# Kernel tuning notes

Measured on AMD Instinct MI355X. Metric: run time of the kernel, lower is better.

Reference implementation:

```python
import jax, jax.numpy as jnp
import numpy as np

NUM_USER = 30000
NUM_ITEM = 30000
N = NUM_USER + NUM_ITEM
DIM = 64          # dim_latent
HID = 4 * DIM     # MLP hidden = 4*dim_latent
E_PAIRS = 500000  # user-item interactions; symmetrized -> 2*E_PAIRS edges
K = 10            # sampling (user-graph neighbors)
B = 2048          # batch_size
DV, DA, DT = 1024, 128, 100


def setup_inputs() -> dict:
    key = jax.random.key(0)
    ks = jax.random.split(key, 24)
    src = jax.random.randint(ks[0], (E_PAIRS,), 0, NUM_USER)
    dst = jax.random.randint(ks[1], (E_PAIRS,), NUM_USER, N)
    # symmetrize like torch.cat((edge, edge[[1,0]]), dim=1)
    edge_index = jnp.stack([jnp.concatenate([src, dst]),
                            jnp.concatenate([dst, src])])  # [2, 2*E_PAIRS]

    def lin_w(k, o, i):
        s = 1.0 / np.sqrt(i)
        return jax.random.uniform(k, (o, i), minval=-s, maxval=s, dtype=jnp.float32)

    return {
        "user_nodes": jax.random.randint(ks[2], (B,), 0, NUM_USER),
        "pos_item_nodes": jax.random.randint(ks[3], (B,), NUM_USER, N),
        "neg_item_nodes": jax.random.randint(ks[4], (B,), NUM_USER, N),
        "user_graph": jax.random.randint(ks[5], (NUM_USER, K), 0, NUM_USER),
        "edge_index": edge_index,
        "user_weight_matrix": jax.nn.softmax(jax.random.normal(ks[6], (NUM_USER, K), dtype=jnp.float32), axis=-1),
        "v_feat": jax.random.normal(ks[7], (NUM_ITEM, DV), dtype=jnp.float32),
        "a_feat": jax.random.normal(ks[8], (NUM_ITEM, DA), dtype=jnp.float32),
        "t_feat": jax.random.normal(ks[9], (NUM_ITEM, DT), dtype=jnp.float32),
        "v_pref": 0.1 * jax.random.normal(ks[10], (NUM_USER, DIM), dtype=jnp.float32),
        "a_pref": 0.1 * jax.random.normal(ks[11], (NUM_USER, DIM), dtype=jnp.float32),
        "t_pref": 0.1 * jax.random.normal(ks[12], (NUM_USER, DIM), dtype=jnp.float32),
        "v_W1": lin_w(ks[13], HID, DV), "v_b1": jnp.zeros((HID,), jnp.float32),
        "v_W2": lin_w(ks[14], DIM, HID), "v_b2": jnp.zeros((DIM,), jnp.float32),
        "a_W1": lin_w(ks[15], HID, DA), "a_b1": jnp.zeros((HID,), jnp.float32),
        "a_W2": lin_w(ks[16], DIM, HID), "a_b2": jnp.zeros((DIM,), jnp.float32),
        "t_W1": lin_w(ks[17], HID, DT), "t_b1": jnp.zeros((HID,), jnp.float32),
        "t_W2": lin_w(ks[18], DIM, HID), "t_b2": jnp.zeros((DIM,), jnp.float32),
        "weight_u": jax.nn.softmax(jax.random.normal(ks[19], (NUM_USER, 3, 1), dtype=jnp.float32), axis=1),
    }


def _l2norm(x):
    # F.normalize(x): rowwise L2 with eps=1e-12
    return x / jnp.maximum(jnp.linalg.norm(x, axis=-1, keepdims=True), 1e-12)


def _gcn_conv(x, src, dst, dinv):
    # Base_gcn(aggr='add'): out[i] = sum_{e: dst_e=i} dinv[src_e]*dinv[dst_e]*x[src_e]
    norm = dinv[src] * dinv[dst]
    return jax.ops.segment_sum(norm[:, None] * x[src], dst, num_segments=N)


def _modality(feat, pref, W1, b1, W2, b2, src, dst, dinv):
    # GCN.forward (Movielens branch, dim_latent=64)
    temp = jax.nn.leaky_relu(feat @ W1.T + b1) @ W2.T + b2  # MLP_1(leaky_relu(MLP(f)))
    x = _l2norm(jnp.concatenate([pref, temp], axis=0))       # [N, DIM]
    h = _gcn_conv(x, src, dst, dinv)
    h1 = _gcn_conv(h, src, dst, dinv)
    return h + x + h1


def reference(user_nodes, pos_item_nodes, neg_item_nodes, user_graph, edge_index,
              user_weight_matrix, v_feat, a_feat, t_feat,
              v_pref, a_pref, t_pref,
              v_W1, v_b1, v_W2, v_b2,
              a_W1, a_b1, a_W2, a_b2,
              t_W1, t_b1, t_W2, t_b2, weight_u):
    src, dst = edge_index[0], edge_index[1]
    deg = jax.ops.segment_sum(jnp.ones_like(src, dtype=jnp.float32), src, num_segments=N)
    dinv = jnp.where(deg > 0, deg ** -0.5, 0.0)

    v_rep = _modality(v_feat, v_pref, v_W1, v_b1, v_W2, v_b2, src, dst, dinv)
    a_rep = _modality(a_feat, a_pref, a_W1, a_b1, a_W2, a_b2, src, dst, dinv)
    t_rep = _modality(t_feat, t_pref, t_W1, t_b1, t_W2, t_b2, src, dst, dinv)

    representation = (v_rep + a_rep + t_rep) / 3.0
    # weighted_sum construction: per-user learned modality weights [U,3,1]
    user_stack = jnp.stack([v_rep[:NUM_USER], a_rep[:NUM_USER], t_rep[:NUM_USER]], axis=2)  # [U, D, 3]
    user_rep = jnp.einsum('udm,umo->ud', user_stack, weight_u)
    item_rep = representation[NUM_USER:]

    # User_Graph_sample: weighted sum over k sampled user neighbors
    h_u1 = jnp.einsum('uk,ukd->ud', user_weight_matrix, user_rep[user_graph])
    user_rep = user_rep + h_u1

    result = jnp.concatenate([user_rep, item_rep], axis=0)  # [N, DIM]
    u = result[user_nodes]
    pos_scores = jnp.sum(u * result[pos_item_nodes], axis=1)
    neg_scores = jnp.sum(u * result[neg_item_nodes], axis=1)
    return pos_scores, neg_scores
```

## Files before the change

kernel.cpp:

```cpp
#include <hip/hip_runtime.h>
#include <hip/hip_bf16.h>
#include <math.h>

#define NUSER 30000
#define NITEM 30000
#define NN    60000
#define NE    1000000
#define DIMV  64
#define XW    192
#define HIDW  256
#define NB    2048
#define KNB   10
#define MPAD  30080
#define NCH   235

typedef __attribute__((ext_vector_type(8))) short bf16x8;
typedef __attribute__((ext_vector_type(4))) float f32x4;

__device__ __forceinline__ short f2bf(float f) {
    union { float f; unsigned u; } v; v.f = f;
    unsigned r = v.u + 0x7fff + ((v.u >> 16) & 1);
    return (short)(r >> 16);
}
__device__ __forceinline__ float bflo(unsigned v) { return __int_as_float(v << 16); }
__device__ __forceinline__ float bfhi(unsigned v) { return __int_as_float(v & 0xffff0000u); }
__device__ __forceinline__ unsigned pack2(float a, float b) {
    return (unsigned)(unsigned short)f2bf(a) | ((unsigned)(unsigned short)f2bf(b) << 16);
}
__device__ __forceinline__ void async16(void* lds, const void* g) {
    __builtin_amdgcn_global_load_lds(
        (const __attribute__((address_space(1))) unsigned*)g,
        (__attribute__((address_space(3))) unsigned*)lds, 16, 0, 0);
}

__global__ void k_deg(const int* __restrict__ src, unsigned* __restrict__ deg) {
    int e = blockIdx.x * blockDim.x + threadIdx.x;
    if (e < NE) atomicAdd(&deg[src[e]], 1u);
}
__global__ void k_dinv(const unsigned* __restrict__ deg, float* __restrict__ dinv) {
    int i = blockIdx.x * blockDim.x + threadIdx.x;
    if (i < NN) { unsigned d = deg[i]; dinv[i] = d ? rsqrtf((float)d) : 0.f; }
}
__global__ __launch_bounds__(256)
void k_bsum(const unsigned* __restrict__ deg, int* __restrict__ bsum) {
    __shared__ int red[4];
    int g = blockIdx.x * 256 + threadIdx.x;
    int v = (g < NN) ? (int)deg[g] : 0;
    for (int o = 32; o > 0; o >>= 1) v += __shfl_down(v, o);
    int lane = threadIdx.x & 63, wave = threadIdx.x >> 6;
    if (lane == 0) red[wave] = v;
    __syncthreads();
    if (threadIdx.x == 0) bsum[blockIdx.x] = red[0] + red[1] + red[2] + red[3];
}
__global__ __launch_bounds__(256)
void k_bscan(const int* __restrict__ bsum, int* __restrict__ bscan) {
    __shared__ int s[256];
    int t = threadIdx.x;
    int v = (t < NCH) ? bsum[t] : 0;
    s[t] = v;
    __syncthreads();
    for (int o = 1; o < 256; o <<= 1) {
        int u = (t >= o) ? s[t - o] : 0;
        __syncthreads();
        s[t] += u;
        __syncthreads();
    }
    if (t < NCH) bscan[t] = s[t] - v;
}
__global__ __launch_bounds__(256)
void k_rowptr(const unsigned* __restrict__ deg, const int* __restrict__ bscan,
              int* __restrict__ rowptr) {
    __shared__ int s[256];
    int g = blockIdx.x * 256 + threadIdx.x, t = threadIdx.x;
    int v = (g < NN) ? (int)deg[g] : 0;
    s[t] = v;
    __syncthreads();
    for (int o = 1; o < 256; o <<= 1) {
        int u = (t >= o) ? s[t - o] : 0;
        __syncthreads();
        s[t] += u;
        __syncthreads();
    }
    int base = bscan[blockIdx.x];
    if (g < NN) rowptr[g] = base + s[t] - v;
    if (g == NN - 1) rowptr[NN] = base + s[t];
}
__global__ void k_fill(const int* __restrict__ src, const int* __restrict__ dst,
                       const float* __restrict__ dinv, const int* __restrict__ rowptr,
                       unsigned* __restrict__ cursor, int2* __restrict__ csr) {
    int e = blockIdx.x * blockDim.x + threadIdx.x;
    if (e >= NE) return;
    int s = src[e], d = dst[e];
    int pos = (int)atomicAdd(&cursor[d], 1u);
    int2 ew;
    ew.x = s;
    ew.y = __float_as_int(dinv[s] * dinv[d]);
    csr[rowptr[d] + pos] = ew;
}

struct CvtArgs { const float* src[9]; short* dst[9]; };
__constant__ __device__ const int C8PRE[10] = {0,3850240,4331520,4812800,4845568,
                                               4849664,4853760,4855808,4857856,4859904};
__constant__ __device__ const int C8SH[9]   = {7,4,4,7,4,4,5,5,5};
__constant__ __device__ const int C8COLS[9] = {1024,128,100,1024,128,100,256,256,256};
__constant__ __device__ const int C8ROWS[9] = {30000,30000,30000,256,256,256,64,64,64};
#define CVT8_TOTAL 4859904

__global__ __launch_bounds__(256)
void k_convert(CvtArgs a) {
    int cid = blockIdx.x * 256 + threadIdx.x;
    if (cid >= CVT8_TOTAL) return;
    int j = 0;
    while (cid >= C8PRE[j + 1]) ++j;
    int local = cid - C8PRE[j];
    int sh = C8SH[j];
    int r = local >> sh;
    int col = (local & ((1 << sh) - 1)) * 8;
    int cols = C8COLS[j];
    bf16x8 o = (bf16x8)0;
    if (r < C8ROWS[j]) {
        const float* s = a.src[j] + (size_t)r * cols + col;
        if (col + 8 <= cols) {
            float4 f0 = *(const float4*)s;
            float4 f1 = *(const float4*)(s + 4);
            o[0] = f2bf(f0.x); o[1] = f2bf(f0.y); o[2] = f2bf(f0.z); o[3] = f2bf(f0.w);
            o[4] = f2bf(f1.x); o[5] = f2bf(f1.y); o[6] = f2bf(f1.z); o[7] = f2bf(f1.w);
        } else {
            #pragma unroll
            for (int q = 0; q < 8; ++q)
                if (col + q < cols) o[q] = f2bf(s[q]);
        }
    }
    *(bf16x8*)(a.dst[j] + ((size_t)r << (sh + 3)) + col) = o;
}

__device__ __forceinline__ bf16x8 ldfrag(const short* lds, int row, int kbyte) {
    int off = (row * 128 + kbyte) ^ ((row & 7) << 4);
    return *(const bf16x8*)((const char*)lds + off);
}
#define STAGE_TILE(SMEM, BASEPTR, LDK, ROWOFF, K0, NITERS)                          \
    _Pragma("unroll")                                                                \
    for (int i_ = 0; i_ < (NITERS); ++i_) {                                          \
        int c_ = i_ * 256 + wave * 64 + lane;                                        \
        int r_ = c_ >> 3, slot_ = c_ & 7;                                            \
        int ss_ = slot_ ^ (r_ & 7);                                                  \
        const char* gp_ = (const char*)((BASEPTR) + (size_t)((ROWOFF) + r_) * (LDK)  \
                                        + (K0)) + ss_ * 16;                          \
        async16(&(SMEM)[(i_ * 256 + wave * 64) * 8], gp_);                           \
    }

struct G1Args { const short* A[3]; const short* W[3]; const float* bias[3];
                short* C[3]; int K[3]; };
__global__ __launch_bounds__(256)
void gemm1_mfma(G1Args g) {
    __shared__ __align__(16) short sA[128 * 64];
    __shared__ __align__(16) short sB[128 * 64];
    int m = blockIdx.z;
    int K = g.K[m];
    const short* A = g.A[m];
    const short* W = g.W[m];
    int lane = threadIdx.x & 63, wave = threadIdx.x >> 6;
    int wr = wave >> 1, wc = wave & 1;
    int lane15 = lane & 15, lhi = lane >> 4;
    int row0 = blockIdx.x * 128, col0 = blockIdx.y * 128;
    f32x4 acc[4][4] = {};
    for (int t = 0; t < (K >> 6); ++t) {
        int k0 = t * 64;
        STAGE_TILE(sA, A, K, row0, k0, 4)
        STAGE_TILE(sB, W, K, col0, k0, 4)
        __syncthreads();
        #pragma unroll
        for (int ks = 0; ks < 2; ++ks) {
            int kb = ks * 64 + lhi * 16;
            bf16x8 a[4], b[4];
            #pragma unroll
            for (int mi = 0; mi < 4; ++mi) a[mi] = ldfrag(sA, wr * 64 + mi * 16 + lane15, kb);
            #pragma unroll
            for (int ni = 0; ni < 4; ++ni) b[ni] = ldfrag(sB, wc * 64 + ni * 16 + lane15, kb);
            #pragma unroll
            for (int mi = 0; mi < 4; ++mi)
                #pragma unroll
                for (int ni = 0; ni < 4; ++ni)
                    acc[mi][ni] = __builtin_amdgcn_mfma_f32_16x16x32_bf16(a[mi], b[ni], acc[mi][ni], 0, 0, 0);
        }
        __syncthreads();
    }
    short* C = g.C[m];
    const float* bias = g.bias[m];
    #pragma unroll
    for (int mi = 0; mi < 4; ++mi) {
        int grow0 = row0 + wr * 64 + mi * 16 + lhi * 4;
        #pragma unroll
        for (int ni = 0; ni < 4; ++ni) {
            int gcol = col0 + wc * 64 + ni * 16 + lane15;
            float bv = bias[gcol];
            #pragma unroll
            for (int r = 0; r < 4; ++r) {
                float v = acc[mi][ni][r] + bv;
                v = v > 0.f ? v : 0.01f * v;
                C[(size_t)(grow0 + r) * HIDW + gcol] = f2bf(v);
            }
        }
    }
}

struct G2Args { const short* A[3]; const short* W[3]; const float* bias[3]; };
__global__ __launch_bounds__(256)
void gemm2_mfma(G2Args g, float* __restrict__ X, short* __restrict__ Xb) {
    __shared__ __align__(16) short sA[128 * 64];
    __shared__ __align__(16) short sB[64 * 64];
    int m = blockIdx.z;
    const short* A = g.A[m];
    const short* W = g.W[m];
    int lane = threadIdx.x & 63, wave = threadIdx.x >> 6;
    int lane15 = lane & 15, lhi = lane >> 4;
    int row0 = blockIdx.x * 128;
    const int K = HIDW;
    f32x4 acc[2][4] = {};
    for (int t = 0; t < 4; ++t) {
        int k0 = t * 64;
        STAGE_TILE(sA, A, K, row0, k0, 4)
        STAGE_TILE(sB, W, K, 0, k0, 2)
        __syncthreads();
        #pragma unroll
        for (int ks = 0; ks < 2; ++ks) {
            int kb = ks * 64 + lhi * 16;
            bf16x8 a[2], b[4];
            #pragma unroll
            for (int mi = 0; mi < 2; ++mi) a[mi] = ldfrag(sA, wave * 32 + mi * 16 + lane15, kb);
            #pragma unroll
            for (int ni = 0; ni < 4; ++ni) b[ni] = ldfrag(sB, ni * 16 + lane15, kb);
            #pragma unroll
            for (int mi = 0; mi < 2; ++mi)
                #pragma unroll
                for (int ni = 0; ni < 4; ++ni)
                    acc[mi][ni] = __builtin_amdgcn_mfma_f32_16x16x32_bf16(a[mi], b[ni], acc[mi][ni], 0, 0, 0);
        }
        __syncthreads();
    }
    const float* bias = g.bias[m];
    #pragma unroll
    for (int mi = 0; mi < 2; ++mi) {
        float v[4][4];
        float sumsq[4] = {};
        #pragma unroll
        for (int ni = 0; ni < 4; ++ni) {
            float bv = bias[ni * 16 + lane15];
            #pragma unroll
            for (int r = 0; r < 4; ++r) {
                float x = acc[mi][ni][r] + bv;
                v[ni][r] = x;
                sumsq[r] += x * x;
            }
        }
        #pragma unroll
        for (int r = 0; r < 4; ++r) {
            float s = sumsq[r];
            s += __shfl_xor(s, 1); s += __shfl_xor(s, 2);
            s += __shfl_xor(s, 4); s += __shfl_xor(s, 8);
            sumsq[r] = 1.f / fmaxf(sqrtf(s), 1e-12f);
        }
        int grow0 = row0 + wave * 32 + mi * 16 + lhi * 4;
        #pragma unroll
        for (int r = 0; r < 4; ++r) {
            int grow = grow0 + r;
            if (grow < NITEM) {
                float sc = sumsq[r];
                size_t o = (size_t)(NUSER + grow) * XW + m * DIMV;
                #pragma unroll
                for (int ni = 0; ni < 4; ++ni) {
                    float val = v[ni][r] * sc;
                    X[o + ni * 16 + lane15] = val;
                    Xb[o + ni * 16 + lane15] = f2bf(val);
                }
            }
        }
    }
}

__global__ void k_users_norm(const float* __restrict__ vp, const float* __restrict__ ap,
                             const float* __restrict__ tp, float* __restrict__ X,
                             short* __restrict__ Xb) {
    int gw = (blockIdx.x * blockDim.x + threadIdx.x) >> 6;
    int lane = threadIdx.x & 63;
    if (gw >= NUSER * 3) return;
    int u = gw / 3, m = gw % 3;
    const float* p = (m == 0) ? vp : (m == 1) ? ap : tp;
    float v = p[(size_t)u * DIMV + lane];
    float s = v * v;
    for (int o = 32; o > 0; o >>= 1) s += __shfl_xor(s, o);
    float sc = 1.f / fmaxf(sqrtf(s), 1e-12f);
    size_t o = (size_t)u * XW + m * DIMV + lane;
    float val = v * sc;
    X[o] = val;
    Xb[o] = f2bf(val);
}

template<int MODE>
__global__ __launch_bounds__(256)
void k_spmm(const int* __restrict__ rowptr, const int2* __restrict__ csr,
            const short* __restrict__ INB, const float* __restrict__ Xf,
            float* __restrict__ OUTf, short* __restrict__ OUTB) {
    int n = blockIdx.x * 4 + (threadIdx.x >> 6);
    int l = threadIdx.x & 63;
    if (n >= NN) return;
    int lo = rowptr[n], hi = rowptr[n + 1];
    int lc = l < 48 ? l : 47;
    float f0 = 0.f, f1 = 0.f, f2 = 0.f, f3 = 0.f;
    for (int base = lo; base < hi; base += 64) {
        int idx = base + l;
        int2 e = (idx < hi) ? csr[idx] : make_int2(0, 0);
        int m = hi - base; if (m > 64) m = 64;
        int j = 0;
        for (; j + 4 <= m; j += 4) {
            int s0 = __builtin_amdgcn_readlane(e.x, j + 0);
            int s1 = __builtin_amdgcn_readlane(e.x, j + 1);
            int s2 = __builtin_amdgcn_readlane(e.x, j + 2);
            int s3 = __builtin_amdgcn_readlane(e.x, j + 3);
            float w0 = __int_as_float(__builtin_amdgcn_readlane(e.y, j + 0));
            float w1 = __int_as_float(__builtin_amdgcn_readlane(e.y, j + 1));
            float w2 = __int_as_float(__builtin_amdgcn_readlane(e.y, j + 2));
            float w3 = __int_as_float(__builtin_amdgcn_readlane(e.y, j + 3));
            uint2 v0 = ((const uint2*)(INB + (size_t)s0 * XW))[lc];
            uint2 v1 = ((const uint2*)(INB + (size_t)s1 * XW))[lc];
            uint2 v2 = ((const uint2*)(INB + (size_t)s2 * XW))[lc];
            uint2 v3 = ((const uint2*)(INB + (size_t)s3 * XW))[lc];
            f0 += w0 * bflo(v0.x); f1 += w0 * bfhi(v0.x);
            f2 += w0 * bflo(v0.y); f3 += w0 * bfhi(v0.y);
            f0 += w1 * bflo(v1.x); f1 += w1 * bfhi(v1.x);
            f2 += w1 * bflo(v1.y); f3 += w1 * bfhi(v1.y);
            f0 += w2 * bflo(v2.x); f1 += w2 * bfhi(v2.x);
            f2 += w2 * bflo(v2.y); f3 += w2 * bfhi(v2.y);
            f0 += w3 * bflo(v3.x); f1 += w3 * bfhi(v3.x);
            f2 += w3 * bflo(v3.y); f3 += w3 * bfhi(v3.y);
        }
        for (; j < m; ++j) {
            int s0 = __builtin_amdgcn_readlane(e.x, j);
            float w0 = __int_as_float(__builtin_amdgcn_readlane(e.y, j));
            uint2 v0 = ((const uint2*)(INB + (size_t)s0 * XW))[lc];
            f0 += w0 * bflo(v0.x); f1 += w0 * bfhi(v0.x);
            f2 += w0 * bflo(v0.y); f3 += w0 * bfhi(v0.y);
        }
    }
    if (MODE == 1) {
        float4 xv = ((const float4*)(Xf + (size_t)n * XW))[lc];
        uint2 hb = ((const uint2*)(INB + (size_t)n * XW))[lc];
        f0 += xv.x + bflo(hb.x); f1 += xv.y + bfhi(hb.x);
        f2 += xv.z + bflo(hb.y); f3 += xv.w + bfhi(hb.y);
    }
    if (l < 48) {
        if (MODE == 0) {
            uint2 ob;
            ob.x = pack2(f0, f1);
            ob.y = pack2(f2, f3);
            ((uint2*)(OUTB + (size_t)n * XW))[l] = ob;
        } else {
            ((float4*)(OUTf + (size_t)n * XW))[l] = make_float4(f0, f1, f2, f3);
        }
    }
}

__global__ void k_combine(const float* __restrict__ REP, const float* __restrict__ wu,
                          float* __restrict__ UR, float* __restrict__ RES) {
    int t = blockIdx.x * blockDim.x + threadIdx.x;
    if (t >= NN * DIMV) return;
    int n = t >> 6, d = t & 63;
    const float* r = REP + (size_t)n * XW;
    float r0 = r[d], r1 = r[DIMV + d], r2 = r[2 * DIMV + d];
    if (n < NUSER) {
        float w0 = wu[n * 3 + 0], w1 = wu[n * 3 + 1], w2 = wu[n * 3 + 2];
        UR[(size_t)n * DIMV + d] = r0 * w0 + r1 * w1 + r2 * w2;
    } else {
        RES[(size_t)n * DIMV + d] = (r0 + r1 + r2) * (1.f / 3.f);
    }
}
__global__ void k_usergraph(const float* __restrict__ UR, const int* __restrict__ g,
                            const float* __restrict__ w, float* __restrict__ RES) {
    int t = blockIdx.x * blockDim.x + threadIdx.x;
    if (t >= NUSER * DIMV) return;
    int n = t >> 6, d = t & 63;
    float acc = UR[(size_t)n * DIMV + d];
    for (int k = 0; k < KNB; ++k) {
        int nb = g[n * KNB + k];
        acc += w[n * KNB + k] * UR[(size_t)nb * DIMV + d];
    }
    RES[(size_t)n * DIMV + d] = acc;
}
__global__ void k_scores(const float* __restrict__ RES, const int* __restrict__ un,
                         const int* __restrict__ pn, const int* __restrict__ nn,
                         float* __restrict__ out) {
    int gw = (blockIdx.x * blockDim.x + threadIdx.x) >> 6;
    int lane = threadIdx.x & 63;
    if (gw >= NB) return;
    int u = un[gw], p = pn[gw], ng = nn[gw];
    float uv = RES[(size_t)u * DIMV + lane];
    float ps = uv * RES[(size_t)p * DIMV + lane];
    float ns = uv * RES[(size_t)ng * DIMV + lane];
    for (int o = 32; o > 0; o >>= 1) {
        ps += __shfl_xor(ps, o);
        ns += __shfl_xor(ns, o);
    }
    if (lane == 0) { out[gw] = ps; out[NB + gw] = ns; }
}

extern "C" void kernel_launch(void* const* d_in, const int* in_sizes, int n_in,
                              void* d_out, int out_size, void* d_ws, size_t ws_size,
                              hipStream_t stream) {
    const int*   un    = (const int*)d_in[0];
    const int*   pn    = (const int*)d_in[1];
    const int*   ngn   = (const int*)d_in[2];
    const int*   ug    = (const int*)d_in[3];
    const int*   eidx  = (const int*)d_in[4];
    const float* uwm   = (const float*)d_in[5];
    const float* feats[3] = { (const float*)d_in[6], (const float*)d_in[7], (const float*)d_in[8] };
    const float* prefs[3] = { (const float*)d_in[9], (const float*)d_in[10], (const float*)d_in[11] };
    const float* W1[3] = { (const float*)d_in[12], (const float*)d_in[16], (const float*)d_in[20] };
    const float* b1[3] = { (const float*)d_in[13], (const float*)d_in[17], (const float*)d_in[21] };
    const float* W2[3] = { (const float*)d_in[14], (const float*)d_in[18], (const float*)d_in[22] };
    const float* b2[3] = { (const float*)d_in[15], (const float*)d_in[19], (const float*)d_in[23] };
    const float* wu    = (const float*)d_in[24];
    float* out = (float*)d_out;

    const int* esrc = eidx;
    const int* edst = eidx + NE;

    char* ws = (char*)d_ws;
    size_t off = 0;
    auto alloc = [&](size_t bytes) { void* p = ws + off; off = (off + bytes + 255) & ~(size_t)255; return p; };
    unsigned* deg    = (unsigned*)alloc(NN * 4);
    float*    dinv   = (float*)alloc(NN * 4);
    int*      rowptr = (int*)alloc((NN + 1) * 4);
    int*      bsum   = (int*)alloc(NCH * 4);
    int*      bscan  = (int*)alloc(NCH * 4);
    int2*     csr    = (int2*)alloc((size_t)NE * 8);
    char* region1 = (char*)alloc((size_t)MPAD * 1280 * 2);
    short* Ab0 = (short*)region1;
    short* Ab1 = (short*)(region1 + (size_t)MPAD * 1024 * 2);
    short* Ab2 = (short*)(region1 + (size_t)MPAD * (1024 + 128) * 2);
    float* X   = (float*)region1;
    short* Xb  = (short*)(region1 + (size_t)NN * XW * 4);
    char* region2 = (char*)alloc((size_t)3 * MPAD * HIDW * 2);
    short* hid[3] = { (short*)region2,
                      (short*)(region2 + (size_t)MPAD * HIDW * 2),
                      (short*)(region2 + (size_t)2 * MPAD * HIDW * 2) };
    float* RES = (float*)region2;
    float* UR  = (float*)(region2 + (size_t)NN * DIMV * 4 + 40960);
    short* Hb  = (short*)(region2 + (size_t)NN * DIMV * 4 + 40960 + (size_t)NUSER * DIMV * 4);
    short* w1b = (short*)alloc((size_t)256 * 1280 * 2);
    short* w1s[3] = { w1b, w1b + 256 * 1024, w1b + 256 * (1024 + 128) };
    short* w2b = (short*)alloc((size_t)3 * 64 * HIDW * 2);
    short* w2s[3] = { w2b, w2b + 64 * HIDW, w2b + 2 * 64 * HIDW };

    CvtArgs ca;
    ca.src[0] = feats[0]; ca.src[1] = feats[1]; ca.src[2] = feats[2];
    ca.src[3] = W1[0];    ca.src[4] = W1[1];    ca.src[5] = W1[2];
    ca.src[6] = W2[0];    ca.src[7] = W2[1];    ca.src[8] = W2[2];
    ca.dst[0] = Ab0; ca.dst[1] = Ab1; ca.dst[2] = Ab2;
    ca.dst[3] = w1s[0]; ca.dst[4] = w1s[1]; ca.dst[5] = w1s[2];
    ca.dst[6] = w2s[0]; ca.dst[7] = w2s[1]; ca.dst[8] = w2s[2];
    k_convert<<<(CVT8_TOTAL + 255) / 256, 256, 0, stream>>>(ca);

    hipMemsetAsync(deg, 0, NN * 4, stream);
    k_deg<<<(NE + 255) / 256, 256, 0, stream>>>(esrc, deg);
    k_dinv<<<(NN + 255) / 256, 256, 0, stream>>>(deg, dinv);
    k_bsum<<<NCH, 256, 0, stream>>>(deg, bsum);
    k_bscan<<<1, 256, 0, stream>>>(bsum, bscan);
    k_rowptr<<<NCH, 256, 0, stream>>>(deg, bscan, rowptr);
    hipMemsetAsync(deg, 0, NN * 4, stream);
    k_fill<<<(NE + 255) / 256, 256, 0, stream>>>(esrc, edst, dinv, rowptr, deg, csr);

    G1Args g1;
    for (int m = 0; m < 3; ++m) { g1.bias[m] = b1[m]; g1.C[m] = hid[m]; g1.W[m] = w1s[m]; }
    g1.A[0] = Ab0; g1.A[1] = Ab1; g1.A[2] = Ab2;
    g1.K[0] = 1024; g1.K[1] = 128; g1.K[2] = 128;
    gemm1_mfma<<<dim3(MPAD / 128, 2, 3), 256, 0, stream>>>(g1);

    G2Args g2;
    for (int m = 0; m < 3; ++m) { g2.A[m] = hid[m]; g2.W[m] = w2s[m]; g2.bias[m] = b2[m]; }
    gemm2_mfma<<<dim3(MPAD / 128, 1, 3), 256, 0, stream>>>(g2, X, Xb);
    k_users_norm<<<(NUSER * 3 * 64 + 255) / 256, 256, 0, stream>>>(prefs[0], prefs[1], prefs[2], X, Xb);

    k_spmm<0><<<(NN + 3) / 4, 256, 0, stream>>>(rowptr, csr, Xb, nullptr, nullptr, Hb);

    k_spmm<1><<<(NN + 3) / 4, 256, 0, stream>>>(rowptr, csr, Hb, X, X, nullptr);

    k_combine<<<(NN * DIMV + 255) / 256, 256, 0, stream>>>(X, wu, UR, RES);
    k_usergraph<<<(NUSER * DIMV + 255) / 256, 256, 0, stream>>>(UR, ug, uwm, RES);
    k_scores<<<(NB * 64 + 255) / 256, 256, 0, stream>>>(RES, un, pn, ngn, out);
}
```

Measured before the change: 350.5 us.

## Fuse fp32-to-bf16 feature conversion into first MLP GEMM with full-width N tile

Stops pre-converting the large item feature matrices to bf16 in a separate pass. The first GEMM now loads fp32 features directly, converts them in registers and writes them into swizzled LDS, with masked loads for the 100-wide text features. The block tile is widened to cover all 256 hidden columns, so each A row is read once instead of twice. This removes one full read and write of the roughly 120 MB visual feature buffer, but uses synchronous global loads instead of async copies and doubles accumulator registers, which may reduce occupancy.

Result: no change. 348.6 us (-0.5%).

```diff
diff --git a/kernel.cpp b/kernel.cpp
--- a/kernel.cpp
+++ b/kernel.cpp
@@ -98,13 +98,12 @@
     csr[rowptr[d] + pos] = ew;
 }
 
-struct CvtArgs { const float* src[9]; short* dst[9]; };
-__constant__ __device__ const int C8PRE[10] = {0,3850240,4331520,4812800,4845568,
-                                               4849664,4853760,4855808,4857856,4859904};
-__constant__ __device__ const int C8SH[9]   = {7,4,4,7,4,4,5,5,5};
-__constant__ __device__ const int C8COLS[9] = {1024,128,100,1024,128,100,256,256,256};
-__constant__ __device__ const int C8ROWS[9] = {30000,30000,30000,256,256,256,64,64,64};
-#define CVT8_TOTAL 4859904
+struct CvtArgs { const float* src[6]; short* dst[6]; };
+__constant__ __device__ const int C8PRE[7]  = {0,32768,36864,40960,43008,45056,47104};
+__constant__ __device__ const int C8SH[6]   = {7,4,4,5,5,5};
+__constant__ __device__ const int C8COLS[6] = {1024,128,100,256,256,256};
+__constant__ __device__ const int C8ROWS[6] = {256,256,256,64,64,64};
+#define CVT8_TOTAL 47104
 
 __global__ __launch_bounds__(256)
 void k_convert(CvtArgs a) {
@@ -149,38 +148,75 @@
         async16(&(SMEM)[(i_ * 256 + wave * 64) * 8], gp_);                           \
     }
 
-struct G1Args { const short* A[3]; const short* W[3]; const float* bias[3];
-                short* C[3]; int K[3]; };
+struct G1Args { const float* A[3]; const short* W[3]; const float* bias[3];
+                short* C[3]; int K[3]; int Ksrc[3]; };
 __global__ __launch_bounds__(256)
 void gemm1_mfma(G1Args g) {
     __shared__ __align__(16) short sA[128 * 64];
-    __shared__ __align__(16) short sB[128 * 64];
+    __shared__ __align__(16) short sB[256 * 64];
     int m = blockIdx.z;
-    int K = g.K[m];
-    const short* A = g.A[m];
+    int K  = g.K[m];
+    int Ks = g.Ksrc[m];
+    const float* A = g.A[m];
     const short* W = g.W[m];
     int lane = threadIdx.x & 63, wave = threadIdx.x >> 6;
     int wr = wave >> 1, wc = wave & 1;
     int lane15 = lane & 15, lhi = lane >> 4;
-    int row0 = blockIdx.x * 128, col0 = blockIdx.y * 128;
-    f32x4 acc[4][4] = {};
+    int row0 = blockIdx.x * 128;
+    int srow = threadIdx.x >> 1, shalf = threadIdx.x & 1;
+    int grow = row0 + srow;
+    bool rowok = grow < NITEM;
+    const float* arow = A + (size_t)grow * Ks + shalf * 32;
+    f32x4 acc[4][8] = {};
     for (int t = 0; t < (K >> 6); ++t) {
         int k0 = t * 64;
-        STAGE_TILE(sA, A, K, row0, k0, 4)
-        STAGE_TILE(sB, W, K, col0, k0, 4)
+        float4 f[8];
+        int gk = k0 + shalf * 32;
+        if (rowok && gk + 32 <= Ks) {
+            #pragma unroll
+            for (int q = 0; q < 8; ++q) f[q] = *(const float4*)(arow + k0 + q * 4);
+        } else {
+            #pragma unroll
+            for (int q = 0; q < 8; ++q) {
+                float4 z = make_float4(0.f, 0.f, 0.f, 0.f);
+                if (rowok) {
+                    int c = gk + q * 4;
+                    if (c + 4 <= Ks) {
+                        z = *(const float4*)(arow + k0 + q * 4);
+                    } else {
+                        if (c + 0 < Ks) z.x = arow[k0 + q * 4 + 0];
+                        if (c + 1 < Ks) z.y = arow[k0 + q * 4 + 1];
+                        if (c + 2 < Ks) z.z = arow[k0 + q * 4 + 2];
+                        if (c + 3 < Ks) z.w = arow[k0 + q * 4 + 3];
+                    }
+                }
+                f[q] = z;
+            }
+        }
+        #pragma unroll
+        for (int q = 0; q < 4; ++q) {
+            bf16x8 o;
+            float4 lo = f[q * 2], hi = f[q * 2 + 1];
+            o[0] = f2bf(lo.x); o[1] = f2bf(lo.y); o[2] = f2bf(lo.z); o[3] = f2bf(lo.w);
+            o[4] = f2bf(hi.x); o[5] = f2bf(hi.y); o[6] = f2bf(hi.z); o[7] = f2bf(hi.w);
+            int c8 = shalf * 4 + q;
+            int off = (srow * 128 + c8 * 16) ^ ((srow & 7) << 4);
+            *(bf16x8*)((char*)sA + off) = o;
+        }
+        STAGE_TILE(sB, W, K, 0, k0, 8)
         __syncthreads();
         #pragma unroll
         for (int ks = 0; ks < 2; ++ks) {
             int kb = ks * 64 + lhi * 16;
-            bf16x8 a[4], b[4];
+            bf16x8 a[4], b[8];
             #pragma unroll
             for (int mi = 0; mi < 4; ++mi) a[mi] = ldfrag(sA, wr * 64 + mi * 16 + lane15, kb);
             #pragma unroll
-            for (int ni = 0; ni < 4; ++ni) b[ni] = ldfrag(sB, wc * 64 + ni * 16 + lane15, kb);
+            for (int ni = 0; ni < 8; ++ni) b[ni] = ldfrag(sB, wc * 128 + ni * 16 + lane15, kb);
             #pragma unroll
             for (int mi = 0; mi < 4; ++mi)
                 #pragma unroll
-                for (int ni = 0; ni < 4; ++ni)
+                for (int ni = 0; ni < 8; ++ni)
                     acc[mi][ni] = __builtin_amdgcn_mfma_f32_16x16x32_bf16(a[mi], b[ni], acc[mi][ni], 0, 0, 0);
         }
         __syncthreads();
@@ -191,8 +227,8 @@
     for (int mi = 0; mi < 4; ++mi) {
         int grow0 = row0 + wr * 64 + mi * 16 + lhi * 4;
         #pragma unroll
-        for (int ni = 0; ni < 4; ++ni) {
-            int gcol = col0 + wc * 64 + ni * 16 + lane15;
+        for (int ni = 0; ni < 8; ++ni) {
+            int gcol = wc * 128 + ni * 16 + lane15;
             float bv = bias[gcol];
             #pragma unroll
             for (int r = 0; r < 4; ++r) {
@@ -433,12 +469,8 @@
     int*      bsum   = (int*)alloc(NCH * 4);
     int*      bscan  = (int*)alloc(NCH * 4);
     int2*     csr    = (int2*)alloc((size_t)NE * 8);
-    char* region1 = (char*)alloc((size_t)MPAD * 1280 * 2);
-    short* Ab0 = (short*)region1;
-    short* Ab1 = (short*)(region1 + (size_t)MPAD * 1024 * 2);
-    short* Ab2 = (short*)(region1 + (size_t)MPAD * (1024 + 128) * 2);
-    float* X   = (float*)region1;
-    short* Xb  = (short*)(region1 + (size_t)NN * XW * 4);
+    float*    X      = (float*)alloc((size_t)NN * XW * 4);
+    short*    Xb     = (short*)alloc((size_t)NN * XW * 2);
     char* region2 = (char*)alloc((size_t)3 * MPAD * HIDW * 2);
     short* hid[3] = { (short*)region2,
                       (short*)(region2 + (size_t)MPAD * HIDW * 2),
@@ -452,12 +484,10 @@
     short* w2s[3] = { w2b, w2b + 64 * HIDW, w2b + 2 * 64 * HIDW };
 
     CvtArgs ca;
-    ca.src[0] = feats[0]; ca.src[1] = feats[1]; ca.src[2] = feats[2];
-    ca.src[3] = W1[0];    ca.src[4] = W1[1];    ca.src[5] = W1[2];
-    ca.src[6] = W2[0];    ca.src[7] = W2[1];    ca.src[8] = W2[2];
-    ca.dst[0] = Ab0; ca.dst[1] = Ab1; ca.dst[2] = Ab2;
-    ca.dst[3] = w1s[0]; ca.dst[4] = w1s[1]; ca.dst[5] = w1s[2];
-    ca.dst[6] = w2s[0]; ca.dst[7] = w2s[1]; ca.dst[8] = w2s[2];
+    ca.src[0] = W1[0]; ca.src[1] = W1[1]; ca.src[2] = W1[2];
+    ca.src[3] = W2[0]; ca.src[4] = W2[1]; ca.src[5] = W2[2];
+    ca.dst[0] = w1s[0]; ca.dst[1] = w1s[1]; ca.dst[2] = w1s[2];
+    ca.dst[3] = w2s[0]; ca.dst[4] = w2s[1]; ca.dst[5] = w2s[2];
     k_convert<<<(CVT8_TOTAL + 255) / 256, 256, 0, stream>>>(ca);
 
     hipMemsetAsync(deg, 0, NN * 4, stream);
@@ -470,10 +500,10 @@
     k_fill<<<(NE + 255) / 256, 256, 0, stream>>>(esrc, edst, dinv, rowptr, deg, csr);
 
     G1Args g1;
-    for (int m = 0; m < 3; ++m) { g1.bias[m] = b1[m]; g1.C[m] = hid[m]; g1.W[m] = w1s[m]; }
-    g1.A[0] = Ab0; g1.A[1] = Ab1; g1.A[2] = Ab2;
+    for (int m = 0; m < 3; ++m) { g1.bias[m] = b1[m]; g1.C[m] = hid[m]; g1.W[m] = w1s[m]; g1.A[m] = feats[m]; }
     g1.K[0] = 1024; g1.K[1] = 128; g1.K[2] = 128;
-    gemm1_mfma<<<dim3(MPAD / 128, 2, 3), 256, 0, stream>>>(g1);
+    g1.Ksrc[0] = 1024; g1.Ksrc[1] = 128; g1.Ksrc[2] = 100;
+    gemm1_mfma<<<dim3(MPAD / 128, 1, 3), 256, 0, stream>>>(g1);
 
     G2Args g2;
     for (int m = 0; m < 3; ++m) { g2.A[m] = hid[m]; g2.W[m] = w2s[m]; g2.bias[m] = b2[m]; }
```
